# Performance work log

Hardware: AMD Instinct MI355X
Metric: run time of the kernel (lower is better)

The kernel has to match this reference:

```python
import jax, jax.numpy as jnp
import numpy as np

B, N, H, HID, LOCALITY = 2, 4096, 4, 256, 30.0
VD = HID // H
F32_MAX = jnp.finfo(jnp.float32).max


def setup_inputs() -> dict:
    key = jax.random.key(0)
    k1, k2, k3, k4 = jax.random.split(key, 4)
    m_dist = jax.random.uniform(k1, (B, N, N), dtype=jnp.float32)  # pairwise distances (b,N,N)
    x = jax.random.normal(k2, (B, N, HID), dtype=jnp.float32)
    r = jax.random.normal(k3, (1, H, 1, 1), dtype=jnp.float32)  # learned per-head distance scale
    # lecun_normal: std = 1/sqrt(fan_in), fan_in = HID
    weight = jax.random.normal(k4, (H, HID, VD), dtype=jnp.float32) / np.sqrt(HID)
    return {"m_dist": m_dist, "x": x, "r": r, "weight": weight}


def reference(m_dist, x, r, weight):
    # scaled distance per head: (b,h,n,n)
    scaled = m_dist[:, None, :, :] * (r ** 2)
    # percentile-thresholded local mask (linear interpolation, per row)
    thresh = jnp.percentile(scaled, LOCALITY, axis=-1, keepdims=True, method="linear")
    scaled = jnp.where(scaled <= thresh, scaled, F32_MAX)
    att = jax.nn.softmax(-scaled, axis=-1)  # (b,h,n,n)
    value = jnp.einsum("bnj,hjk->bhnk", x, weight)  # (b,h,n,v)
    out = jnp.einsum("bhnj,bhjd->bhnd", att, value)  # (b,h,n,v)
    out = jnp.transpose(out, (0, 2, 1, 3)).reshape(out.shape[0], -1, HID)  # (b,n,hid)
    return jax.nn.gelu(out, approximate=False)
```

## Files before the change

### kernel.cpp

```cpp
#include <hip/hip_runtime.h>
#include <hip/hip_bf16.h>

#define Bc   2
#define Nc   4096
#define Hc   4
#define HIDc 256
#define VDc  64

typedef short s8v  __attribute__((ext_vector_type(8)));
typedef float f4v  __attribute__((ext_vector_type(4)));

__global__ __launch_bounds__(256) void value_kernel(
    const float* __restrict__ x, const float* __restrict__ wgt,
    unsigned short* __restrict__ vt_g)
{
    __shared__ float xs[64 * HIDc];
    __shared__ unsigned short ob[64 * 64];

    int t  = threadIdx.x;
    int bid = blockIdx.x;
    int nt = bid & 63;
    int h  = (bid >> 6) & 3;
    int b  = bid >> 8;
    int n0 = nt * 64;

    const float* xg = x + ((size_t)b * Nc + n0) * HIDc;
    #pragma unroll
    for (int i = 0; i < 16; i++)
        ((float4*)xs)[t + i * 256] = ((const float4*)xg)[t + i * 256];
    __syncthreads();

    int k4 = t & 15;
    int ns = t >> 4;
    const float4* wg4 = (const float4*)(wgt + (size_t)h * HIDc * VDc);

    float acc[4][4];
    #pragma unroll
    for (int i = 0; i < 4; i++)
        #pragma unroll
        for (int c = 0; c < 4; c++) acc[i][c] = 0.0f;

    for (int j = 0; j < HIDc; j++) {
        float4 wv = wg4[j * 16 + k4];
        #pragma unroll
        for (int i = 0; i < 4; i++) {
            float xv = xs[(ns + i * 16) * HIDc + j];
            acc[i][0] += xv * wv.x;
            acc[i][1] += xv * wv.y;
            acc[i][2] += xv * wv.z;
            acc[i][3] += xv * wv.w;
        }
    }
    #pragma unroll
    for (int i = 0; i < 4; i++) {
        int nn = ns + i * 16;
        #pragma unroll
        for (int c = 0; c < 4; c++) {
            __hip_bfloat16 hb = __float2bfloat16(acc[i][c]);
            ob[(k4 * 4 + c) * 64 + nn] = *(unsigned short*)&hb;
        }
    }
    __syncthreads();

    unsigned short* vg = vt_g + (((size_t)b * Hc + h) * VDc) * Nc + n0;
    #pragma unroll
    for (int i = 0; i < 16; i++) {
        int idx = t + i * 256;
        int kk = idx >> 6, nn = idx & 63;
        vg[(size_t)kk * Nc + nn] = ob[idx];
    }
}

__global__ __launch_bounds__(256) void thresh_kernel(
    const float* __restrict__ m_dist,
    float* __restrict__ thr_out, float* __restrict__ min_out)
{
    __shared__ unsigned int hist[1024];
    __shared__ float wred[4];
    __shared__ unsigned int wscan[4];
    __shared__ int b0s, b1s;
    __shared__ unsigned int c0s;
    __shared__ unsigned int ncand;
    __shared__ float cand[256];
    __shared__ float s0s, s1s;

    int t = threadIdx.x;
    size_t rowid = blockIdx.x;
    const float* row = m_dist + rowid * Nc;

    for (int i = t; i < 1024; i += 256) hist[i] = 0u;
    if (t == 0) ncand = 0u;
    __syncthreads();

    float4 vals[4];
    float lmin = 1e30f;
    #pragma unroll
    for (int i = 0; i < 4; i++) {
        float4 v = ((const float4*)row)[t + i * 256];
        vals[i] = v;
        lmin = fminf(lmin, fminf(fminf(v.x, v.y), fminf(v.z, v.w)));
        atomicAdd(&hist[min(1023, (int)(v.x * 1024.0f))], 1u);
        atomicAdd(&hist[min(1023, (int)(v.y * 1024.0f))], 1u);
        atomicAdd(&hist[min(1023, (int)(v.z * 1024.0f))], 1u);
        atomicAdd(&hist[min(1023, (int)(v.w * 1024.0f))], 1u);
    }
    #pragma unroll
    for (int o = 32; o > 0; o >>= 1) lmin = fminf(lmin, __shfl_xor(lmin, o));
    if ((t & 63) == 0) wred[t >> 6] = lmin;
    __syncthreads();
    float rmin = fminf(fminf(wred[0], wred[1]), fminf(wred[2], wred[3]));

    unsigned int c[4], csum = 0;
    #pragma unroll
    for (int j = 0; j < 4; j++) { c[j] = hist[t * 4 + j]; csum += c[j]; }
    unsigned int inc = csum;
    #pragma unroll
    for (int o = 1; o < 64; o <<= 1) {
        unsigned int nv = __shfl_up(inc, o);
        if ((t & 63) >= o) inc += nv;
    }
    if ((t & 63) == 63) wscan[t >> 6] = inc;
    __syncthreads();
    unsigned int wpref = 0;
    for (int wv = 0; wv < (t >> 6); wv++) wpref += wscan[wv];
    unsigned int P = wpref + inc - csum;

    const unsigned int R0 = 1228u, R1 = 1229u;
    unsigned int cum = P;
    #pragma unroll
    for (int j = 0; j < 4; j++) {
        unsigned int lo = cum, hi = cum + c[j];
        if (R0 >= lo && R0 < hi) { b0s = t * 4 + j; c0s = lo; }
        if (R1 >= lo && R1 < hi) { b1s = t * 4 + j; }
        cum = hi;
    }
    __syncthreads();
    int b0 = b0s, b1 = b1s;
    unsigned int C0 = c0s;

    #pragma unroll
    for (int i = 0; i < 4; i++) {
        float a[4] = {vals[i].x, vals[i].y, vals[i].z, vals[i].w};
        #pragma unroll
        for (int j = 0; j < 4; j++) {
            int bx = min(1023, (int)(a[j] * 1024.0f));
            if (bx >= b0 && bx <= b1) {
                unsigned int p = atomicAdd(&ncand, 1u);
                if (p < 256u) cand[p] = a[j];
            }
        }
    }
    __syncthreads();
    unsigned int nc = min(ncand, 256u);
    if ((unsigned int)t < nc) {
        float v = cand[t];
        unsigned int rk = C0;
        for (unsigned int j = 0; j < nc; j++) {
            float u = cand[j];
            rk += (u < v || (u == v && j < (unsigned int)t)) ? 1u : 0u;
        }
        if (rk == R0) s0s = v;
        if (rk == R1) s1s = v;
    }
    __syncthreads();
    if (t == 0) {
        thr_out[rowid] = 0.5f * (s0s + s1s);
        min_out[rowid] = rmin;
    }
}

#define NT 32
#define JT 64
#define MPAD 68
#define WPAD 72

__global__ __launch_bounds__(512, 6) void attn_kernel(
    const float* __restrict__ m_dist, const float* __restrict__ rr,
    const unsigned short* __restrict__ vt_g,
    const float* __restrict__ thr_g, const float* __restrict__ min_g,
    float* __restrict__ Op, float* __restrict__ Zp, int jlen)
{
    __shared__ float ms[NT * MPAD];
    __shared__ unsigned short vt[Hc * VDc * WPAD];

    int t = threadIdx.x;
    const int nblk = Bc * (Nc / NT);
    int js = blockIdx.x / nblk;
    int rb = blockIdx.x - js * nblk;
    int b  = rb >> 7;
    int n0 = (rb & 127) * NT;
    int j0 = js * jlen;

    int lane = t & 63, q = lane >> 4, m16 = lane & 15;
    int w = t >> 6;
    int h = w & 3, rh = w >> 2;
    int row = rh * 16 + m16;

    float th = thr_g[b * Nc + n0 + row];
    float mn = min_g[b * Nc + n0 + row];
    float rv = rr[h];
    float cc = -(rv * rv) * 1.4426950408889634f;

    f4v acc[4];
    #pragma unroll
    for (int ct = 0; ct < 4; ct++) acc[ct] = (f4v){0.f, 0.f, 0.f, 0.f};
    float zacc = 0.f;

    const float* mbase = m_dist + ((size_t)b * Nc + n0) * Nc + j0;
    const unsigned short* vtb = vt_g + ((size_t)b * Hc * VDc) * Nc + j0;

    for (int jt = 0; jt < jlen; jt += JT) {
        {
            int r_ = t >> 4, ch = t & 15;
            *(float4*)&ms[r_ * MPAD + ch * 4] =
                *(const float4*)(mbase + (size_t)r_ * Nc + jt + ch * 4);
        }
        #pragma unroll
        for (int i = 0; i < 4; i++) {
            int cid = t + i * 512;
            int rrow = cid >> 3, ch = cid & 7;
            *(float4*)&vt[rrow * WPAD + ch * 8] =
                *(const float4*)(vtb + (size_t)rrow * Nc + jt + ch * 8);
        }
        __syncthreads();

        const unsigned short* vb = &vt[(h * VDc) * WPAD];
        #pragma unroll
        for (int ks = 0; ks < 2; ks++) {
            float4 a0 = *(const float4*)&ms[row * MPAD + ks * 32 + q * 8];
            float4 a1 = *(const float4*)&ms[row * MPAD + ks * 32 + q * 8 + 4];
            float w0 = (a0.x <= th) ? __builtin_amdgcn_exp2f((a0.x - mn) * cc) : 0.f;
            float w1 = (a0.y <= th) ? __builtin_amdgcn_exp2f((a0.y - mn) * cc) : 0.f;
            float w2 = (a0.z <= th) ? __builtin_amdgcn_exp2f((a0.z - mn) * cc) : 0.f;
            float w3 = (a0.w <= th) ? __builtin_amdgcn_exp2f((a0.w - mn) * cc) : 0.f;
            float w4 = (a1.x <= th) ? __builtin_amdgcn_exp2f((a1.x - mn) * cc) : 0.f;
            float w5 = (a1.y <= th) ? __builtin_amdgcn_exp2f((a1.y - mn) * cc) : 0.f;
            float w6 = (a1.z <= th) ? __builtin_amdgcn_exp2f((a1.z - mn) * cc) : 0.f;
            float w7 = (a1.w <= th) ? __builtin_amdgcn_exp2f((a1.w - mn) * cc) : 0.f;
            zacc += ((w0 + w1) + (w2 + w3)) + ((w4 + w5) + (w6 + w7));
            union { unsigned short s[8]; s8v v; } afu;
            __hip_bfloat16 hb;
            hb = __float2bfloat16(w0); afu.s[0] = *(unsigned short*)&hb;
            hb = __float2bfloat16(w1); afu.s[1] = *(unsigned short*)&hb;
            hb = __float2bfloat16(w2); afu.s[2] = *(unsigned short*)&hb;
            hb = __float2bfloat16(w3); afu.s[3] = *(unsigned short*)&hb;
            hb = __float2bfloat16(w4); afu.s[4] = *(unsigned short*)&hb;
            hb = __float2bfloat16(w5); afu.s[5] = *(unsigned short*)&hb;
            hb = __float2bfloat16(w6); afu.s[6] = *(unsigned short*)&hb;
            hb = __float2bfloat16(w7); afu.s[7] = *(unsigned short*)&hb;
            #pragma unroll
            for (int ct = 0; ct < 4; ct++) {
                s8v bf = *(const s8v*)(vb + (ct * 16 + m16) * WPAD + ks * 32 + q * 8);
                acc[ct] = __builtin_amdgcn_mfma_f32_16x16x32_bf16(afu.v, bf, acc[ct], 0, 0, 0);
            }
        }
        __syncthreads();
    }

    zacc += __shfl_xor(zacc, 16);
    zacc += __shfl_xor(zacc, 32);
    if (q == 0)
        Zp[(((size_t)js * Bc + b) * Hc + h) * Nc + n0 + row] = zacc;

    #pragma unroll
    for (int ct = 0; ct < 4; ct++) {
        #pragma unroll
        for (int rg = 0; rg < 4; rg++) {
            int nl = rh * 16 + q * 4 + rg;
            Op[(((size_t)js * Bc + b) * Nc + n0 + nl) * HIDc + h * VDc + ct * 16 + m16]
                = acc[ct][rg];
        }
    }
}

__global__ __launch_bounds__(256) void combine_kernel(
    const float* __restrict__ Op, const float* __restrict__ Zp,
    float* __restrict__ out, int S)
{
    int g = blockIdx.x * 256 + threadIdx.x;
    int c4 = g & 63;
    int n  = (g >> 6) & (Nc - 1);
    int b  = g >> 18;
    int h  = c4 >> 4;

    float z = 0.f;
    float4 v = {0.f, 0.f, 0.f, 0.f};
    for (int s = 0; s < S; s++) {
        z += Zp[(((size_t)s * Bc + b) * Hc + h) * Nc + n];
        float4 p = *(const float4*)&Op[(((size_t)s * Bc + b) * Nc + n) * HIDc + c4 * 4];
        v.x += p.x; v.y += p.y; v.z += p.z; v.w += p.w;
    }
    float iz = 1.0f / z;
    float4 o;
    float u;
    u = v.x * iz; o.x = 0.5f * u * (1.0f + erff(u * 0.7071067811865476f));
    u = v.y * iz; o.y = 0.5f * u * (1.0f + erff(u * 0.7071067811865476f));
    u = v.z * iz; o.z = 0.5f * u * (1.0f + erff(u * 0.7071067811865476f));
    u = v.w * iz; o.w = 0.5f * u * (1.0f + erff(u * 0.7071067811865476f));
    *(float4*)&out[(((size_t)b * Nc + n) * HIDc) + c4 * 4] = o;
}

extern "C" void kernel_launch(void* const* d_in, const int* in_sizes, int n_in,
                              void* d_out, int out_size, void* d_ws, size_t ws_size,
                              hipStream_t stream) {
    const float* m_dist = (const float*)d_in[0];
    const float* x      = (const float*)d_in[1];
    const float* r      = (const float*)d_in[2];
    const float* weight = (const float*)d_in[3];
    float* out = (float*)d_out;

    char* ws = (char*)d_ws;
    const size_t MB = 1024 * 1024;
    unsigned short* vt = (unsigned short*)ws;
    float* thr = (float*)(ws + 4 * MB);
    float* mn  = (float*)(ws + 4 * MB + 32 * 1024);
    float* Zp  = (float*)(ws + 4 * MB + 64 * 1024);
    float* Op  = (float*)(ws + 5 * MB);

    int S = 4;
    if (ws_size < 5 * MB + 4 * (size_t)(Bc * Nc * HIDc * 4)) S = 2;
    if (ws_size < 5 * MB + 2 * (size_t)(Bc * Nc * HIDc * 4)) S = 1;
    int jlen = Nc / S;

    value_kernel<<<512, 256, 0, stream>>>(x, weight, vt);
    thresh_kernel<<<Bc * Nc, 256, 0, stream>>>(m_dist, thr, mn);
    attn_kernel<<<S * Bc * (Nc / NT), 512, 0, stream>>>(m_dist, r, vt, thr, mn, Op, Zp, jlen);
    combine_kernel<<<(Bc * Nc * HIDc) / 1024, 256, 0, stream>>>(Op, Zp, out, S);
}
```

Baseline: 296.0 us.

## Prefetch next tile into registers in attention loop and pad value-kernel LDS

The attention kernel's main loop now holds the next m_dist and value tiles in registers, loading them right after the barrier so global loads overlap with the exp/MFMA compute instead of stalling at the top of each iteration. Separately, the value projection kernel pads its shared x tile to 260 floats per row and reads four x values as a float4 per step, with four weight rows per iteration, which cuts LDS bank conflicts and load instructions. The prefetch raises register pressure in the attention kernel, which could reduce occupancy.

Measured after the change: 381.8 us. 29.0% more time.

```diff
diff --git a/kernel.cpp b/kernel.cpp
--- a/kernel.cpp
+++ b/kernel.cpp
@@ -10,11 +10,13 @@
 typedef short s8v  __attribute__((ext_vector_type(8)));
 typedef float f4v  __attribute__((ext_vector_type(4)));
 
+#define XSP 260
+
 __global__ __launch_bounds__(256) void value_kernel(
     const float* __restrict__ x, const float* __restrict__ wgt,
     unsigned short* __restrict__ vt_g)
 {
-    __shared__ float xs[64 * HIDc];
+    __shared__ float xs[64 * XSP];
     __shared__ unsigned short ob[64 * 64];
 
     int t  = threadIdx.x;
@@ -26,37 +28,42 @@
 
     const float* xg = x + ((size_t)b * Nc + n0) * HIDc;
     #pragma unroll
-    for (int i = 0; i < 16; i++)
-        ((float4*)xs)[t + i * 256] = ((const float4*)xg)[t + i * 256];
+    for (int i = 0; i < 16; i++) {
+        int id = t + i * 256;
+        int row = id >> 6, ch = id & 63;
+        *(float4*)&xs[row * XSP + ch * 4] = ((const float4*)xg)[id];
+    }
     __syncthreads();
 
     int k4 = t & 15;
     int ns = t >> 4;
     const float4* wg4 = (const float4*)(wgt + (size_t)h * HIDc * VDc);
 
-    float acc[4][4];
-    #pragma unroll
-    for (int i = 0; i < 4; i++)
-        #pragma unroll
-        for (int c = 0; c < 4; c++) acc[i][c] = 0.0f;
-
-    for (int j = 0; j < HIDc; j++) {
-        float4 wv = wg4[j * 16 + k4];
+    float4 acc[4];
+    #pragma unroll
+    for (int i = 0; i < 4; i++) acc[i] = (float4){0.f, 0.f, 0.f, 0.f};
+
+    for (int j = 0; j < HIDc; j += 4) {
+        float4 w0 = wg4[(j + 0) * 16 + k4];
+        float4 w1 = wg4[(j + 1) * 16 + k4];
+        float4 w2 = wg4[(j + 2) * 16 + k4];
+        float4 w3 = wg4[(j + 3) * 16 + k4];
         #pragma unroll
         for (int i = 0; i < 4; i++) {
-            float xv = xs[(ns + i * 16) * HIDc + j];
-            acc[i][0] += xv * wv.x;
-            acc[i][1] += xv * wv.y;
-            acc[i][2] += xv * wv.z;
-            acc[i][3] += xv * wv.w;
+            float4 xv = *(const float4*)&xs[(ns + i * 16) * XSP + j];
+            acc[i].x += xv.x * w0.x + xv.y * w1.x + xv.z * w2.x + xv.w * w3.x;
+            acc[i].y += xv.x * w0.y + xv.y * w1.y + xv.z * w2.y + xv.w * w3.y;
+            acc[i].z += xv.x * w0.z + xv.y * w1.z + xv.z * w2.z + xv.w * w3.z;
+            acc[i].w += xv.x * w0.w + xv.y * w1.w + xv.z * w2.w + xv.w * w3.w;
         }
     }
     #pragma unroll
     for (int i = 0; i < 4; i++) {
         int nn = ns + i * 16;
+        float a[4] = {acc[i].x, acc[i].y, acc[i].z, acc[i].w};
         #pragma unroll
         for (int c = 0; c < 4; c++) {
-            __hip_bfloat16 hb = __float2bfloat16(acc[i][c]);
+            __hip_bfloat16 hb = __float2bfloat16(a[c]);
             ob[(k4 * 4 + c) * 64 + nn] = *(unsigned short*)&hb;
         }
     }
@@ -209,20 +216,29 @@
     const float* mbase = m_dist + ((size_t)b * Nc + n0) * Nc + j0;
     const unsigned short* vtb = vt_g + ((size_t)b * Hc * VDc) * Nc + j0;
 
+    int mrow = t >> 4, mch = t & 15;
+    const float* mptr = mbase + (size_t)mrow * Nc + mch * 4;
+    int vrow0 = t >> 3, vch = t & 7;
+
+    float4 pm = *(const float4*)(mptr);
+    float4 pv[4];
+    #pragma unroll
+    for (int i = 0; i < 4; i++)
+        pv[i] = *(const float4*)(vtb + (size_t)(vrow0 + i * 64) * Nc + vch * 8);
+
     for (int jt = 0; jt < jlen; jt += JT) {
-        {
-            int r_ = t >> 4, ch = t & 15;
-            *(float4*)&ms[r_ * MPAD + ch * 4] =
-                *(const float4*)(mbase + (size_t)r_ * Nc + jt + ch * 4);
-        }
-        #pragma unroll
-        for (int i = 0; i < 4; i++) {
-            int cid = t + i * 512;
-            int rrow = cid >> 3, ch = cid & 7;
-            *(float4*)&vt[rrow * WPAD + ch * 8] =
-                *(const float4*)(vtb + (size_t)rrow * Nc + jt + ch * 8);
-        }
+        *(float4*)&ms[mrow * MPAD + mch * 4] = pm;
+        #pragma unroll
+        for (int i = 0; i < 4; i++)
+            *(float4*)&vt[(vrow0 + i * 64) * WPAD + vch * 8] = pv[i];
         __syncthreads();
+
+        if (jt + JT < jlen) {
+            pm = *(const float4*)(mptr + jt + JT);
+            #pragma unroll
+            for (int i = 0; i < 4; i++)
+                pv[i] = *(const float4*)(vtb + (size_t)(vrow0 + i * 64) * Nc + (jt + JT) + vch * 8);
+        }
 
         const unsigned short* vb = &vt[(h * VDc) * WPAD];
         #pragma unroll
```
